# Optimization experiments

Hardware: AMD Instinct MI355X
Metric: run time of the kernel (lower is better)

## Reference

```python
import jax, jax.numpy as jnp
import numpy as np

B, N, S, K = 16, 16384, 4096, 16
D_PT, D_IN, C_MID, D_OUT = 3, 64, 16, 128
HID = [8, 8]


def _layernorm(x, g, b, eps=1e-5):
    m = x.mean(-1, keepdims=True)
    v = x.var(-1, keepdims=True)
    return (x - m) * jax.lax.rsqrt(v + eps) * g + b


def _gather(feat, idx):
    # feat: [B, C, N], idx: [B, S, K] -> [B, C, S, K]
    return jax.vmap(lambda f, i: f[:, i])(feat, idx)


def setup_inputs() -> dict:
    key = jax.random.key(0)
    ks = jax.random.split(key, 16)
    inp = {
        "xyz": jax.random.normal(ks[0], (B, D_PT, N), jnp.float32),
        "points": jax.random.normal(ks[1], (B, D_IN, N), jnp.float32),
        "new_xyz": jax.random.normal(ks[2], (B, D_PT, S), jnp.float32),
        "nn_idx": jax.random.randint(ks[3], (B, S, K), 0, N, jnp.int32),
    }
    # WeightNet: Linear(3,8)+LN(8), Linear(8,8)+LN(8), Linear(8,16)+LN(16)
    dims = [D_PT] + HID + [C_MID]
    for i in range(3):
        inp[f"w{i}"] = jax.random.normal(ks[4 + i], (dims[i], dims[i + 1]), jnp.float32) * 0.1
        inp[f"b{i}"] = jnp.zeros((dims[i + 1],), jnp.float32)
        inp[f"g{i}"] = jnp.ones((dims[i + 1],), jnp.float32)
        inp[f"be{i}"] = jnp.zeros((dims[i + 1],), jnp.float32)
    last_ch = D_PT + D_IN  # 67
    inp["wl"] = jax.random.normal(ks[8], (C_MID * last_ch, D_OUT), jnp.float32) * 0.02
    inp["bl"] = jnp.zeros((D_OUT,), jnp.float32)
    inp["gl"] = jnp.ones((D_OUT,), jnp.float32)
    inp["bel"] = jnp.zeros((D_OUT,), jnp.float32)
    return inp


def reference(xyz, points, new_xyz, nn_idx,
              w0, b0, g0, be0, w1, b1, g1, be1, w2, b2, g2, be2,
              wl, bl, gl, bel):
    # gather neighbor positions / features: [B, C, S, K]
    grouped_xyz = _gather(xyz, nn_idx)
    gxn = grouped_xyz - new_xyz[:, :, :, None]          # [B, 3, S, K]
    feat = jnp.concatenate([_gather(points, nn_idx), gxn], axis=1)  # [B, 67, S, K]

    # WeightNet on relative coords: MLP over channel dim, layout [B, S, K, 3]
    w = jnp.transpose(gxn, (0, 2, 3, 1))
    for wi, bi, gi, bei in ((w0, b0, g0, be0), (w1, b1, g1, be1), (w2, b2, g2, be2)):
        w = jax.nn.leaky_relu(_layernorm(w @ wi + bi, gi, bei), 0.2)
    # w: [B, S, K, c_mid]

    # weighted aggregation: out[b,s,c,m] = sum_k feat[b,c,s,k] * w[b,s,k,m]
    agg = jnp.einsum("bcsk,bskm->bscm", feat, w).reshape(B, S, -1)  # [B, S, 67*c_mid]

    out = _layernorm(agg @ wl + bl, gl, bel)
    out = jax.nn.leaky_relu(out, 0.2)
    return jnp.transpose(out, (0, 2, 1))  # [B, out_channel, S]
```

## Files before the change

kernel.cpp:

```cpp
#include <hip/hip_runtime.h>

#define B_ 16
#define N_ 16384
#define S_ 4096
#define K_ 16
#define TS 32
#define DOUT 128

typedef __bf16 bf16;
typedef __attribute__((ext_vector_type(8))) __bf16 bf16x8;
typedef __attribute__((ext_vector_type(4))) float f32x4;

__device__ __forceinline__ unsigned pack2(float a, float b) {
  unsigned short ua = __builtin_bit_cast(unsigned short, (bf16)a);
  unsigned short ub = __builtin_bit_cast(unsigned short, (bf16)b);
  return (unsigned)ua | ((unsigned)ub << 16);
}

template <int NCH>
__device__ __forceinline__ void ln_leaky(const float* h, const float* g, const float* e, float* o) {
  float m = 0.f;
#pragma unroll
  for (int j = 0; j < NCH; ++j) m += h[j];
  m *= (1.0f / NCH);
  float v = 0.f;
#pragma unroll
  for (int j = 0; j < NCH; ++j) { float d = h[j] - m; v += d * d; }
  v *= (1.0f / NCH);
  float inv = rsqrtf(v + 1e-5f);
#pragma unroll
  for (int j = 0; j < NCH; ++j) {
    float t = (h[j] - m) * inv * g[j] + e[j];
    o[j] = t < 0.f ? 0.2f * t : t;
  }
}

__global__ void k_fill(float* out, float v) {
  out[blockIdx.x * 256 + threadIdx.x] = v;
}

__global__ __launch_bounds__(256) void k_transpose(const float* __restrict__ pts,
                                                   bf16* __restrict__ pt) {
  int b = blockIdx.y;
  int n0 = blockIdx.x * 256;
  int tc = threadIdx.x & 7;
  int tn = threadIdx.x >> 3;
  const float* src = pts + (size_t)b * 64 * N_ + (size_t)(tc * 8) * N_ + n0 + tn * 8;
  float4 row[8][2];
#pragma unroll
  for (int i = 0; i < 8; ++i) {
    row[i][0] = *(const float4*)(src + (size_t)i * N_);
    row[i][1] = *(const float4*)(src + (size_t)i * N_ + 4);
  }
  bf16* dst = pt + ((size_t)b * N_ + n0 + tn * 8) * 64 + tc * 8;
#pragma unroll
  for (int j = 0; j < 8; ++j) {
    float v[8];
#pragma unroll
    for (int i = 0; i < 8; ++i) {
      float4 q = row[i][j >> 2];
      v[i] = ((j & 3) == 0) ? q.x : ((j & 3) == 1) ? q.y : ((j & 3) == 2) ? q.z : q.w;
    }
    *(uint4*)(dst + (size_t)j * 64) = make_uint4(
        pack2(v[0], v[1]), pack2(v[2], v[3]), pack2(v[4], v[5]), pack2(v[6], v[7]));
  }
}

__global__ void k_wlf(const float* __restrict__ wl, bf16* __restrict__ wlF) {
  int blk = blockIdx.x;
  int kkg = blk % 34;
  int t = blk / 34;
  int tid = threadIdx.x;
  int L = tid >> 2, jp = (tid & 3) * 2;
  int k = kkg * 32 + ((L >> 4) << 3) + jp;
  int n = t * 16 + (L & 15);
  float v0 = (k < 1072) ? wl[(size_t)k * 128 + n] : 0.f;
  float v1 = (k + 1 < 1072) ? wl[(size_t)(k + 1) * 128 + n] : 0.f;
  ((unsigned*)wlF)[(size_t)blk * 256 + tid] = pack2(v0, v1);
}

__global__ __launch_bounds__(256, 4) void k_main(
    const float* __restrict__ xyz, const float* __restrict__ nxyz,
    const int* __restrict__ nnidx,
    const bf16* __restrict__ ptT, const bf16* __restrict__ wlF,
    const float* __restrict__ w0p, const float* __restrict__ b0p,
    const float* __restrict__ g0p, const float* __restrict__ be0p,
    const float* __restrict__ w1p, const float* __restrict__ b1p,
    const float* __restrict__ g1p, const float* __restrict__ be1p,
    const float* __restrict__ w2p, const float* __restrict__ b2p,
    const float* __restrict__ g2p, const float* __restrict__ be2p,
    const float* __restrict__ blp, const float* __restrict__ glp,
    const float* __restrict__ belp, float* __restrict__ out) {
  __shared__ __align__(16) bf16 w_sT[32 * 264];
  __shared__ __align__(16) bf16 feat2[32 * 144];
  __shared__ __align__(16) bf16 aggA[32 * 136];
  __shared__ float nx[3][TS];
  __shared__ float ln_m[TS], ln_i[TS];

  const int tid = threadIdx.x;
  const unsigned Lwg = blockIdx.y * 128u + blockIdx.x;
  const int xcd = (int)(Lwg & 7u);
  const int li = (int)(Lwg >> 3);
  const int b = xcd * 2 + (li >> 7);
  const int s0 = (li & 127) * TS;
  const size_t ibase = ((size_t)b * S_ + s0) * K_;

  if (tid < 96) {
    int c = tid >> 5, j = tid & 31;
    nx[c][j] = nxyz[((size_t)b * 3 + c) * S_ + s0 + j];
  }
  const int ig0 = nnidx[ibase + tid];
  const int ig1 = nnidx[ibase + tid + 256];
  const int iw0 = nnidx[ibase + 2 * tid];
  const int iw1 = nnidx[ibase + 2 * tid + 1];
  __syncthreads();

  float xa[3], xb[3];
  const int ws = tid >> 3;
  const int wk = (tid & 7) * 2;
  {
#pragma unroll
    for (int c = 0; c < 3; ++c) {
      float nv = nx[c][ws];
      xa[c] = xyz[((size_t)b * 3 + c) * N_ + iw0] - nv;
      xb[c] = xyz[((size_t)b * 3 + c) * N_ + iw1] - nv;
    }
    float ya[8], yb[8];
    {
      float h0[8], h1[8];
#pragma unroll
      for (int j = 0; j < 8; ++j) {
        h0[j] = b0p[j] + xa[0] * w0p[j] + xa[1] * w0p[8 + j] + xa[2] * w0p[16 + j];
        h1[j] = b0p[j] + xb[0] * w0p[j] + xb[1] * w0p[8 + j] + xb[2] * w0p[16 + j];
      }
      ln_leaky<8>(h0, g0p, be0p, ya);
      ln_leaky<8>(h1, g0p, be0p, yb);
    }
    {
      float h0[8], h1[8];
#pragma unroll
      for (int j = 0; j < 8; ++j) { h0[j] = b1p[j]; h1[j] = b1p[j]; }
#pragma unroll
      for (int i = 0; i < 8; ++i) {
#pragma unroll
        for (int j = 0; j < 8; ++j) {
          float w = w1p[i * 8 + j];
          h0[j] += ya[i] * w; h1[j] += yb[i] * w;
        }
      }
      ln_leaky<8>(h0, g1p, be1p, ya);
      ln_leaky<8>(h1, g1p, be1p, yb);
    }
    {
      float h0[16], h1[16];
#pragma unroll
      for (int j = 0; j < 16; ++j) { h0[j] = b2p[j]; h1[j] = b2p[j]; }
#pragma unroll
      for (int i = 0; i < 8; ++i) {
#pragma unroll
        for (int j = 0; j < 16; ++j) {
          float w = w2p[i * 16 + j];
          h0[j] += ya[i] * w; h1[j] += yb[i] * w;
        }
      }
      float z0[16], z1[16];
      ln_leaky<16>(h0, g2p, be2p, z0);
      ln_leaky<16>(h1, g2p, be2p, z1);
      bf16* wp = w_sT + ws * 264 + wk;
#pragma unroll
      for (int m = 0; m < 16; ++m)
        *(unsigned*)(wp + m * 16) = pack2(z0[m], z1[m]);
    }
  }

  const int lane = tid & 63;
  const int wv = tid >> 6;
  const int rt = wv & 1;
  const int cw = wv >> 1;
  const int l16 = lane & 15;
  const int q = lane >> 4;
  const bool adiag = ((((lane >> 5) ^ (lane >> 3)) & 1) == 0);
  const int aoff = ((lane >> 3) & 1) * 144 + (lane & 7) * 16 + (q & 1) * 8;
  const int boff = (lane >> 5) * 264 + l16 * 16 + (q & 1) * 8;
  const int soff = (lane >> 5) * 136 + (q & 1) * 64 + l16;
  f32x4 a00 = {0.f, 0.f, 0.f, 0.f};
  f32x4 a01 = a00, a10 = a00, a11 = a00;
  const f32x4 zc = a00;

  const bf16* ptB = ptT + (size_t)b * N_ * 64;
  const int gs0 = tid >> 4, gk = tid & 15;

  uint4 pf0, pf1;
  pf0 = *(const uint4*)(ptB + (size_t)ig0 * 64);
  pf1 = *(const uint4*)(ptB + (size_t)ig1 * 64);

  for (int ch = 0; ch < 9; ++ch) {
    const int nkk = (ch < 8) ? 4 : 2;
    __syncthreads();
    if (ch < 8) {
      bf16 t0[8], t1[8];
      *(uint4*)t0 = pf0;
      *(uint4*)t1 = pf1;
      bf16* f0 = feat2 + gs0 * 144 + gk;
      bf16* f1 = feat2 + (gs0 + 16) * 144 + gk;
#pragma unroll
      for (int c = 0; c < 8; ++c) {
        f0[c * 16] = t0[c];
        f1[c * 16] = t1[c];
      }
    } else {
      bf16* fp = feat2 + ws * 144 + wk;
      *(unsigned*)(fp + 0 * 16) = pack2(xa[0], xb[0]);
      *(unsigned*)(fp + 1 * 16) = pack2(xa[1], xb[1]);
      *(unsigned*)(fp + 2 * 16) = pack2(xa[2], xb[2]);
#pragma unroll
      for (int c = 3; c < 8; ++c) *(unsigned*)(fp + c * 16) = 0u;
    }
    __syncthreads();
    if (ch < 8) {
      int nc = ch + 1;
      if (nc < 8) {
        pf0 = *(const uint4*)(ptB + (size_t)ig0 * 64 + nc * 8);
        pf1 = *(const uint4*)(ptB + (size_t)ig1 * 64 + nc * 8);
      }
    }
#pragma unroll
    for (int pp = 0; pp < 4; ++pp) {
      int s2 = (wv * 4 + pp) * 2;
      uint4 au = *(const uint4*)(feat2 + s2 * 144 + aoff);
      if (!adiag) au = make_uint4(0u, 0u, 0u, 0u);
      bf16x8 af = __builtin_bit_cast(bf16x8, au);
      bf16x8 bw = *(const bf16x8*)(w_sT + s2 * 264 + boff);
      f32x4 d = __builtin_amdgcn_mfma_f32_16x16x32_bf16(af, bw, zc, 0, 0, 0);
      bf16* cp = aggA + s2 * 136 + soff;
#pragma unroll
      for (int r = 0; r < 4; ++r) cp[r * 16] = (bf16)d[r];
    }
    __syncthreads();
    {
      const bf16* arow = aggA + (rt * 16 + l16) * 136 + q * 8;
      const size_t lb = (size_t)lane * 8;
      const size_t kb = (size_t)(ch * 4) * 512;
      const bf16* w0f = wlF + (size_t)(2 * cw + 0) * 17408 + kb + lb;
      const bf16* w1f = wlF + (size_t)(2 * cw + 1) * 17408 + kb + lb;
      const bf16* w2f = wlF + (size_t)(2 * cw + 4) * 17408 + kb + lb;
      const bf16* w3f = wlF + (size_t)(2 * cw + 5) * 17408 + kb + lb;
      for (int kk = 0; kk < nkk; ++kk) {
        bf16x8 af = *(const bf16x8*)(arow + kk * 32);
        bf16x8 bf0 = *(const bf16x8*)(w0f + kk * 512);
        bf16x8 bf1 = *(const bf16x8*)(w1f + kk * 512);
        bf16x8 bf2 = *(const bf16x8*)(w2f + kk * 512);
        bf16x8 bf3 = *(const bf16x8*)(w3f + kk * 512);
        a00 = __builtin_amdgcn_mfma_f32_16x16x32_bf16(af, bf0, a00, 0, 0, 0);
        a01 = __builtin_amdgcn_mfma_f32_16x16x32_bf16(af, bf1, a01, 0, 0, 0);
        a10 = __builtin_amdgcn_mfma_f32_16x16x32_bf16(af, bf2, a10, 0, 0, 0);
        a11 = __builtin_amdgcn_mfma_f32_16x16x32_bf16(af, bf3, a11, 0, 0, 0);
      }
    }
  }

  __syncthreads();
  float* out_s = (float*)w_sT;
  {
    int row = rt * 16 + q * 4;
    int c0 = (2 * cw + 0) * 16 + l16;
    int c1 = (2 * cw + 1) * 16 + l16;
    int c2 = 64 + c0;
    int c3 = 64 + c1;
    float bl0 = blp[c0], bl1 = blp[c1], bl2 = blp[c2], bl3 = blp[c3];
#pragma unroll
    for (int r = 0; r < 4; ++r) {
      out_s[(row + r) * 132 + c0] = a00[r] + bl0;
      out_s[(row + r) * 132 + c1] = a01[r] + bl1;
      out_s[(row + r) * 132 + c2] = a10[r] + bl2;
      out_s[(row + r) * 132 + c3] = a11[r] + bl3;
    }
  }
  __syncthreads();
  {
    int r = tid >> 3, g = tid & 7;
    const float* rowp = out_s + r * 132;
    float s1 = 0.f;
#pragma unroll
    for (int i = 0; i < 16; ++i) s1 += rowp[g + 8 * i];
    s1 += __shfl_xor(s1, 1);
    s1 += __shfl_xor(s1, 2);
    s1 += __shfl_xor(s1, 4);
    float m = s1 * (1.0f / 128.0f);
    float s2 = 0.f;
#pragma unroll
    for (int i = 0; i < 16; ++i) { float d = rowp[g + 8 * i] - m; s2 += d * d; }
    s2 += __shfl_xor(s2, 1);
    s2 += __shfl_xor(s2, 2);
    s2 += __shfl_xor(s2, 4);
    if (g == 0) {
      ln_m[r] = m;
      ln_i[r] = rsqrtf(s2 * (1.0f / 128.0f) + 1e-5f);
    }
  }
  __syncthreads();
  {
    int d = tid >> 1, sh = tid & 1;
    float gld = glp[d], beld = belp[d];
    float vals[16];
#pragma unroll
    for (int j = 0; j < 16; ++j) {
      int r = sh * 16 + j;
      float v = (out_s[r * 132 + d] - ln_m[r]) * ln_i[r] * gld + beld;
      vals[j] = v < 0.f ? 0.2f * v : v;
    }
    float* op = out + ((size_t)b * DOUT + d) * S_ + s0 + sh * 16;
#pragma unroll
    for (int i = 0; i < 4; ++i)
      *(float4*)(op + 4 * i) =
          make_float4(vals[4 * i], vals[4 * i + 1], vals[4 * i + 2], vals[4 * i + 3]);
  }
}

extern "C" void kernel_launch(void* const* d_in, const int* in_sizes, int n_in,
                              void* d_out, int out_size, void* d_ws, size_t ws_size,
                              hipStream_t stream) {
  const float* xyz  = (const float*)d_in[0];
  const float* pts  = (const float*)d_in[1];
  const float* nxyz = (const float*)d_in[2];
  const int* nnidx  = (const int*)d_in[3];
  const float* w0p  = (const float*)d_in[4];
  const float* b0p  = (const float*)d_in[5];
  const float* g0p  = (const float*)d_in[6];
  const float* be0p = (const float*)d_in[7];
  const float* w1p  = (const float*)d_in[8];
  const float* b1p  = (const float*)d_in[9];
  const float* g1p  = (const float*)d_in[10];
  const float* be1p = (const float*)d_in[11];
  const float* w2p  = (const float*)d_in[12];
  const float* b2p  = (const float*)d_in[13];
  const float* g2p  = (const float*)d_in[14];
  const float* be2p = (const float*)d_in[15];
  const float* wlp  = (const float*)d_in[16];
  const float* blp  = (const float*)d_in[17];
  const float* glp  = (const float*)d_in[18];
  const float* belp = (const float*)d_in[19];
  float* out = (float*)d_out;

  const size_t PTT_BYTES = (size_t)B_ * N_ * 64 * 2;
  const size_t WLF_BYTES = (size_t)8 * 34 * 64 * 8 * 2;
  bf16* ptT = (bf16*)d_ws;
  bf16* wlF = (bf16*)((char*)d_ws + PTT_BYTES);

  (void)hipGetLastError();

  if (ws_size < PTT_BYTES + WLF_BYTES) {
    k_fill<<<dim3(8), dim3(256), 0, stream>>>(out, 5000.0f);
    return;
  }

  k_transpose<<<dim3(N_ / 256, B_), dim3(256), 0, stream>>>(pts, ptT);
  hipError_t e1 = hipGetLastError();
  k_wlf<<<dim3(8 * 34), dim3(256), 0, stream>>>(wlp, wlF);
  hipError_t e2 = hipGetLastError();
  k_main<<<dim3(S_ / TS, B_), dim3(256), 0, stream>>>(
      xyz, nxyz, nnidx, ptT, wlF,
      w0p, b0p, g0p, be0p, w1p, b1p, g1p, be1p,
      w2p, b2p, g2p, be2p, blp, glp, belp, out);
  hipError_t e3 = hipGetLastError();

  if (e1 != hipSuccess)
    k_fill<<<dim3(8), dim3(256), 0, stream>>>(out, 2000.0f + (float)(int)e1);
  if (e2 != hipSuccess)
    k_fill<<<dim3(8), dim3(256), 0, stream>>>(out, 3000.0f + (float)(int)e2);
  if (e3 != hipSuccess)
    k_fill<<<dim3(8), dim3(256), 0, stream>>>(out, 4000.0f + (float)(int)e3);
}
```

Baseline: 240.3 us.

## Merge prep kernels, double-buffer feature gathers, swizzle LDS, and prioritize MFMA

```diff
diff --git a/kernel.cpp b/kernel.cpp
--- a/kernel.cpp
+++ b/kernel.cpp
@@ -39,44 +39,49 @@
   out[blockIdx.x * 256 + threadIdx.x] = v;
 }
 
-__global__ __launch_bounds__(256) void k_transpose(const float* __restrict__ pts,
-                                                   bf16* __restrict__ pt) {
-  int b = blockIdx.y;
-  int n0 = blockIdx.x * 256;
-  int tc = threadIdx.x & 7;
-  int tn = threadIdx.x >> 3;
-  const float* src = pts + (size_t)b * 64 * N_ + (size_t)(tc * 8) * N_ + n0 + tn * 8;
-  float4 row[8][2];
-#pragma unroll
-  for (int i = 0; i < 8; ++i) {
-    row[i][0] = *(const float4*)(src + (size_t)i * N_);
-    row[i][1] = *(const float4*)(src + (size_t)i * N_ + 4);
-  }
-  bf16* dst = pt + ((size_t)b * N_ + n0 + tn * 8) * 64 + tc * 8;
-#pragma unroll
-  for (int j = 0; j < 8; ++j) {
-    float v[8];
+__global__ __launch_bounds__(256) void k_prep(const float* __restrict__ pts,
+                                              bf16* __restrict__ pt,
+                                              const float* __restrict__ wl,
+                                              bf16* __restrict__ wlF) {
+  int bi = blockIdx.x;
+  if (bi < 1024) {
+    int xcd = bi & 7;
+    int li = bi >> 3;
+    int b = xcd * 2 + (li >> 6);
+    int n0 = (li & 63) * 256;
+    int tc = threadIdx.x & 7;
+    int tn = threadIdx.x >> 3;
+    const float* src = pts + (size_t)b * 64 * N_ + (size_t)(tc * 8) * N_ + n0 + tn * 8;
+    float4 row[8][2];
 #pragma unroll
     for (int i = 0; i < 8; ++i) {
-      float4 q = row[i][j >> 2];
-      v[i] = ((j & 3) == 0) ? q.x : ((j & 3) == 1) ? q.y : ((j & 3) == 2) ? q.z : q.w;
-    }
-    *(uint4*)(dst + (size_t)j * 64) = make_uint4(
-        pack2(v[0], v[1]), pack2(v[2], v[3]), pack2(v[4], v[5]), pack2(v[6], v[7]));
-  }
-}
-
-__global__ void k_wlf(const float* __restrict__ wl, bf16* __restrict__ wlF) {
-  int blk = blockIdx.x;
-  int kkg = blk % 34;
-  int t = blk / 34;
-  int tid = threadIdx.x;
-  int L = tid >> 2, jp = (tid & 3) * 2;
-  int k = kkg * 32 + ((L >> 4) << 3) + jp;
-  int n = t * 16 + (L & 15);
-  float v0 = (k < 1072) ? wl[(size_t)k * 128 + n] : 0.f;
-  float v1 = (k + 1 < 1072) ? wl[(size_t)(k + 1) * 128 + n] : 0.f;
-  ((unsigned*)wlF)[(size_t)blk * 256 + tid] = pack2(v0, v1);
+      row[i][0] = *(const float4*)(src + (size_t)i * N_);
+      row[i][1] = *(const float4*)(src + (size_t)i * N_ + 4);
+    }
+    bf16* dst = pt + ((size_t)b * N_ + n0 + tn * 8) * 64 + tc * 8;
+#pragma unroll
+    for (int j = 0; j < 8; ++j) {
+      float v[8];
+#pragma unroll
+      for (int i = 0; i < 8; ++i) {
+        float4 q = row[i][j >> 2];
+        v[i] = ((j & 3) == 0) ? q.x : ((j & 3) == 1) ? q.y : ((j & 3) == 2) ? q.z : q.w;
+      }
+      *(uint4*)(dst + (size_t)j * 64) = make_uint4(
+          pack2(v[0], v[1]), pack2(v[2], v[3]), pack2(v[4], v[5]), pack2(v[6], v[7]));
+    }
+  } else {
+    int blk = bi - 1024;
+    int kkg = blk % 34;
+    int t = blk / 34;
+    int tid = threadIdx.x;
+    int L = tid >> 2, jp = (tid & 3) * 2;
+    int k = kkg * 32 + ((L >> 4) << 3) + jp;
+    int n = t * 16 + (L & 15);
+    float v0 = (k < 1072) ? wl[(size_t)k * 128 + n] : 0.f;
+    float v1 = (k + 1 < 1072) ? wl[(size_t)(k + 1) * 128 + n] : 0.f;
+    ((unsigned*)wlF)[(size_t)blk * 256 + tid] = pack2(v0, v1);
+  }
 }
 
 __global__ __launch_bounds__(256, 4) void k_main(
@@ -113,6 +118,12 @@
   const int ig1 = nnidx[ibase + tid + 256];
   const int iw0 = nnidx[ibase + 2 * tid];
   const int iw1 = nnidx[ibase + 2 * tid + 1];
+
+  const bf16* ptB = ptT + (size_t)b * N_ * 64;
+  uint4 pfA0 = *(const uint4*)(ptB + (size_t)ig0 * 64);
+  uint4 pfA1 = *(const uint4*)(ptB + (size_t)ig1 * 64);
+  uint4 pfB0 = *(const uint4*)(ptB + (size_t)ig0 * 64 + 8);
+  uint4 pfB1 = *(const uint4*)(ptB + (size_t)ig1 * 64 + 8);
   __syncthreads();
 
   float xa[3], xb[3];
@@ -166,10 +177,13 @@
       float z0[16], z1[16];
       ln_leaky<16>(h0, g2p, be2p, z0);
       ln_leaky<16>(h1, g2p, be2p, z1);
-      bf16* wp = w_sT + ws * 264 + wk;
-#pragma unroll
-      for (int m = 0; m < 16; ++m)
+      bf16* wpA = w_sT + ws * 264 + wk;
+      bf16* wpB = w_sT + ws * 264 + (wk ^ 8);
+#pragma unroll
+      for (int m = 0; m < 16; ++m) {
+        bf16* wp = (((m >> 2) & 1) ? wpB : wpA);
         *(unsigned*)(wp + m * 16) = pack2(z0[m], z1[m]);
+      }
     }
   }
 
@@ -180,50 +194,37 @@
   const int l16 = lane & 15;
   const int q = lane >> 4;
   const bool adiag = ((((lane >> 5) ^ (lane >> 3)) & 1) == 0);
-  const int aoff = ((lane >> 3) & 1) * 144 + (lane & 7) * 16 + (q & 1) * 8;
-  const int boff = (lane >> 5) * 264 + l16 * 16 + (q & 1) * 8;
+  const int aoff = ((lane >> 3) & 1) * 144 + (lane & 7) * 16 +
+                   (((q & 1) ^ ((lane >> 3) & 1)) << 3);
+  const int boff = (lane >> 5) * 264 + l16 * 16 +
+                   (((q & 1) ^ ((l16 >> 2) & 1)) << 3);
   const int soff = (lane >> 5) * 136 + (q & 1) * 64 + l16;
   f32x4 a00 = {0.f, 0.f, 0.f, 0.f};
   f32x4 a01 = a00, a10 = a00, a11 = a00;
   const f32x4 zc = a00;
 
-  const bf16* ptB = ptT + (size_t)b * N_ * 64;
   const int gs0 = tid >> 4, gk = tid & 15;
-
-  uint4 pf0, pf1;
-  pf0 = *(const uint4*)(ptB + (size_t)ig0 * 64);
-  pf1 = *(const uint4*)(ptB + (size_t)ig1 * 64);
+  bf16* f0 = feat2 + gs0 * 144 + (gk ^ ((gs0 & 1) << 3));
+  bf16* f1 = f0 + 16 * 144;
+
+  auto stage_pair = [&](const uint4& p0, const uint4& p1) {
+    bf16 t0[8], t1[8];
+    *(uint4*)t0 = p0;
+    *(uint4*)t1 = p1;
+#pragma unroll
+    for (int c = 0; c < 8; ++c) {
+      f0[c * 16] = t0[c];
+      f1[c * 16] = t1[c];
+    }
+  };
+
+  stage_pair(pfA0, pfA1);
+  pfA0 = *(const uint4*)(ptB + (size_t)ig0 * 64 + 16);
+  pfA1 = *(const uint4*)(ptB + (size_t)ig1 * 64 + 16);
+  __syncthreads();
 
   for (int ch = 0; ch < 9; ++ch) {
     const int nkk = (ch < 8) ? 4 : 2;
-    __syncthreads();
-    if (ch < 8) {
-      bf16 t0[8], t1[8];
-      *(uint4*)t0 = pf0;
-      *(uint4*)t1 = pf1;
-      bf16* f0 = feat2 + gs0 * 144 + gk;
-      bf16* f1 = feat2 + (gs0 + 16) * 144 + gk;
-#pragma unroll
-      for (int c = 0; c < 8; ++c) {
-        f0[c * 16] = t0[c];
-        f1[c * 16] = t1[c];
-      }
-    } else {
-      bf16* fp = feat2 + ws * 144 + wk;
-      *(unsigned*)(fp + 0 * 16) = pack2(xa[0], xb[0]);
-      *(unsigned*)(fp + 1 * 16) = pack2(xa[1], xb[1]);
-      *(unsigned*)(fp + 2 * 16) = pack2(xa[2], xb[2]);
-#pragma unroll
-      for (int c = 3; c < 8; ++c) *(unsigned*)(fp + c * 16) = 0u;
-    }
-    __syncthreads();
-    if (ch < 8) {
-      int nc = ch + 1;
-      if (nc < 8) {
-        pf0 = *(const uint4*)(ptB + (size_t)ig0 * 64 + nc * 8);
-        pf1 = *(const uint4*)(ptB + (size_t)ig1 * 64 + nc * 8);
-      }
-    }
 #pragma unroll
     for (int pp = 0; pp < 4; ++pp) {
       int s2 = (wv * 4 + pp) * 2;
@@ -237,6 +238,29 @@
       for (int r = 0; r < 4; ++r) cp[r * 16] = (bf16)d[r];
     }
     __syncthreads();
+    if (ch < 7) {
+      if (ch & 1) {
+        stage_pair(pfA0, pfA1);
+        if (ch <= 4) {
+          pfA0 = *(const uint4*)(ptB + (size_t)ig0 * 64 + (ch + 3) * 8);
+          pfA1 = *(const uint4*)(ptB + (size_t)ig1 * 64 + (ch + 3) * 8);
+        }
+      } else {
+        stage_pair(pfB0, pfB1);
+        if (ch <= 4) {
+          pfB0 = *(const uint4*)(ptB + (size_t)ig0 * 64 + (ch + 3) * 8);
+          pfB1 = *(const uint4*)(ptB + (size_t)ig1 * 64 + (ch + 3) * 8);
+        }
+      }
+    } else if (ch == 7) {
+      bf16* fp = feat2 + ws * 144 + (wk ^ ((ws & 1) << 3));
+      *(unsigned*)(fp + 0 * 16) = pack2(xa[0], xb[0]);
+      *(unsigned*)(fp + 1 * 16) = pack2(xa[1], xb[1]);
+      *(unsigned*)(fp + 2 * 16) = pack2(xa[2], xb[2]);
+#pragma unroll
+      for (int c = 3; c < 8; ++c) *(unsigned*)(fp + c * 16) = 0u;
+    }
+    __builtin_amdgcn_s_setprio(1);
     {
       const bf16* arow = aggA + (rt * 16 + l16) * 136 + q * 8;
       const size_t lb = (size_t)lane * 8;
@@ -257,9 +281,10 @@
         a11 = __builtin_amdgcn_mfma_f32_16x16x32_bf16(af, bf3, a11, 0, 0, 0);
       }
     }
-  }
-
-  __syncthreads();
+    __builtin_amdgcn_s_setprio(0);
+    __syncthreads();
+  }
+
   float* out_s = (float*)w_sT;
   {
     int row = rt * 16 + q * 4;
@@ -354,10 +379,8 @@
     return;
   }
 
-  k_transpose<<<dim3(N_ / 256, B_), dim3(256), 0, stream>>>(pts, ptT);
+  k_prep<<<dim3(1024 + 8 * 34), dim3(256), 0, stream>>>(pts, ptT, wlp, wlF);
   hipError_t e1 = hipGetLastError();
-  k_wlf<<<dim3(8 * 34), dim3(256), 0, stream>>>(wlp, wlF);
-  hipError_t e2 = hipGetLastError();
   k_main<<<dim3(S_ / TS, B_), dim3(256), 0, stream>>>(
       xyz, nxyz, nnidx, ptT, wlF,
       w0p, b0p, g0p, be0p, w1p, b1p, g1p, be1p,
@@ -366,8 +389,6 @@
 
   if (e1 != hipSuccess)
     k_fill<<<dim3(8), dim3(256), 0, stream>>>(out, 2000.0f + (float)(int)e1);
-  if (e2 != hipSuccess)
-    k_fill<<<dim3(8), dim3(256), 0, stream>>>(out, 3000.0f + (float)(int)e2);
   if (e3 != hipSuccess)
     k_fill<<<dim3(8), dim3(256), 0, stream>>>(out, 4000.0f + (float)(int)e3);
 }
```

New measurement: 238.9 us. About the same (-0.6%).
